# Kernel tuning notes

Measured on AMD Instinct MI355X. Metric: run time of the kernel, lower is better.

## Reference

```python
import jax, jax.numpy as jnp
import numpy as np

D_MODEL = 512
NUM_HEADS = 8
D_K = D_MODEL // NUM_HEADS


def setup_inputs() -> dict:
    key = jax.random.key(0)
    ks = jax.random.split(key, 12)
    B, Sq, Sk = 4, 2048, 2048
    scale = 1.0 / np.sqrt(D_MODEL)
    inp = {
        'query': jax.random.normal(ks[0], (B, Sq, D_MODEL), jnp.float32),
        'key':   jax.random.normal(ks[1], (B, Sk, D_MODEL), jnp.float32),
        'value': jax.random.normal(ks[2], (B, Sk, D_MODEL), jnp.float32),
        'wq': jax.random.normal(ks[3], (D_MODEL, D_MODEL), jnp.float32) * scale,
        'bq': jnp.zeros((D_MODEL,), jnp.float32),
        'wk': jax.random.normal(ks[4], (D_MODEL, D_MODEL), jnp.float32) * scale,
        'bk': jnp.zeros((D_MODEL,), jnp.float32),
        'wv': jax.random.normal(ks[5], (D_MODEL, D_MODEL), jnp.float32) * scale,
        'bv': jnp.zeros((D_MODEL,), jnp.float32),
        'wo': jax.random.normal(ks[6], (D_MODEL, D_MODEL), jnp.float32) * scale,
        'bo': jnp.zeros((D_MODEL,), jnp.float32),
        'ln_g': jnp.ones((D_MODEL,), jnp.float32),
        'ln_b': jnp.zeros((D_MODEL,), jnp.float32),
    }
    return inp


def _layer_norm(x, g, b, eps=1e-5):
    mu = jnp.mean(x, axis=-1, keepdims=True)
    var = jnp.mean(jnp.square(x - mu), axis=-1, keepdims=True)
    return (x - mu) * jax.lax.rsqrt(var + eps) * g + b


def reference(query, key, value, wq, bq, wk, bk, wv, bv, wo, bo, ln_g, ln_b):
    B, Sq, _ = query.shape
    Sk = key.shape[1]
    residual = query
    # projections: torch Linear computes x @ W^T + b; here wq is (out,in)-free:
    # we store weights as (d_model, d_model) and use x @ W + b (equivalent param space)
    Q = (query @ wq + bq).reshape(B, Sq, NUM_HEADS, D_K).transpose(0, 2, 1, 3)
    K = (key   @ wk + bk).reshape(B, Sk, NUM_HEADS, D_K).transpose(0, 2, 1, 3)
    V = (value @ wv + bv).reshape(B, Sk, NUM_HEADS, D_K).transpose(0, 2, 1, 3)
    scores = jnp.einsum('bhqd,bhkd->bhqk', Q, K) / jnp.sqrt(jnp.float32(D_K))
    attn = jax.nn.softmax(scores, axis=-1)  # dropout is identity in eval
    context = jnp.einsum('bhqk,bhkd->bhqd', attn, V)
    context = context.transpose(0, 2, 1, 3).reshape(B, Sq, D_MODEL)
    out = context @ wo + bo
    return _layer_norm(out + residual, ln_g, ln_b)
```

## Files before the change

kernel.cpp:

```cpp
#include <hip/hip_runtime.h>
#include <cstdint>
#include <cstddef>

typedef unsigned short u16;
typedef __bf16 bf16x8 __attribute__((ext_vector_type(8)));
typedef __bf16 bf16x4 __attribute__((ext_vector_type(4)));
typedef float f32x4 __attribute__((ext_vector_type(4)));

#define DEVI __device__ __forceinline__

DEVI u16 f2bf(float f){
  union { float f; unsigned u; } v; v.f = f;
  unsigned r = v.u + 0x7fffu + ((v.u >> 16) & 1u);
  return (u16)(r >> 16);
}

#if defined(__has_builtin)
#if __has_builtin(__builtin_amdgcn_exp2f)
#define EXP2F(x) __builtin_amdgcn_exp2f(x)
#else
#define EXP2F(x) exp2f(x)
#endif
#else
#define EXP2F(x) exp2f(x)
#endif

#define MFMA16(a,b,c) __builtin_amdgcn_mfma_f32_16x16x32_bf16((a),(b),(c),0,0,0)

DEVI void gload_lds16(const void* g, void* l){
  __builtin_amdgcn_global_load_lds(
      (const __attribute__((address_space(1))) void*)g,
      (__attribute__((address_space(3))) void*)l, 16, 0, 0);
}

#define BARRIER do{ __builtin_amdgcn_s_barrier(); \
    __builtin_amdgcn_sched_barrier(0); }while(0)


__global__ void k_prep_w(const float* __restrict__ w0, const float* __restrict__ w1,
                         const float* __restrict__ w2, const float* __restrict__ w3,
                         u16* __restrict__ wt){
  __shared__ u16 tile[64][72];
  int p = blockIdx.z;
  const float* W = (p==0)?w0:((p==1)?w1:((p==2)?w2:w3));
  int k0 = blockIdx.x*64, n0 = blockIdx.y*64;
  int t = threadIdx.x;
  int tr = t >> 4, tc = t & 15;
  #pragma unroll
  for (int pass=0; pass<4; pass++){
    int row = pass*16 + tr;
    float4 a = *(const float4*)(W + (size_t)(k0+row)*512 + n0 + tc*4);
    tile[row][tc*4+0] = f2bf(a.x);
    tile[row][tc*4+1] = f2bf(a.y);
    tile[row][tc*4+2] = f2bf(a.z);
    tile[row][tc*4+3] = f2bf(a.w);
  }
  __syncthreads();
  #pragma unroll
  for (int pass=0; pass<4; pass++){
    int n = pass*16 + tr;
    ushort4 o;
    o.x = tile[tc*4+0][n];
    o.y = tile[tc*4+1][n];
    o.z = tile[tc*4+2][n];
    o.w = tile[tc*4+3][n];
    *(ushort4*)(wt + (size_t)p*262144 + (size_t)(n0+n)*512 + k0 + tc*4) = o;
  }
}

__global__ __launch_bounds__(256)
void k_gemm_qkv(const float* __restrict__ xq, const float* __restrict__ xk,
                const float* __restrict__ xv, const u16* __restrict__ wt,
                const float* __restrict__ bq, const float* __restrict__ bk,
                const float* __restrict__ bv,
                u16* __restrict__ qb, u16* __restrict__ kb, u16* __restrict__ vt){
  int l = threadIdx.x & 63, w = threadIdx.x >> 6;
  int lr = l & 15, lg = l >> 4;
  int f = blockIdx.x;
  int xcd = f & 7, j0 = f >> 3;
  int pm   = xcd*24 + (j0 >> 2);
  int nblk = j0 & 3;
  int p    = pm >> 6, mblk = pm & 63;
  int wr = w >> 1, wc = w & 1;

  const float* bias = (p==0)?bq:((p==1)?bk:bv);
  float osc = (p==0)? (0.125f*1.44269504088896340736f) : 1.0f;

  const float* Ag32 = ((p==0)?xq:((p==1)?xk:xv)) + (size_t)mblk*128*512;
  const char*  Bg   = (const char*)(wt + (size_t)p*262144 + (size_t)nblk*128*512);

  __shared__ __align__(16) u16 Albuf[2][8192];
  __shared__ __align__(16) u16 Blbuf[2][8192];

  int r8 = l >> 3, sl = l & 7;
  int ar = w*8 + r8;
  int as = sl;

  float4 av[8];
  #define A_ISSUE(tt) do{ \
    _Pragma("unroll") \
    for (int p4=0; p4<4; ++p4){ \
      int r = ar + p4*32; \
      const float* src = Ag32 + (size_t)r*512 + (tt)*64 + as*8; \
      av[p4*2]   = *(const float4*)src; \
      av[p4*2+1] = *(const float4*)(src+4); \
    } }while(0)

  #define A_WRITE(buf) do{ \
    _Pragma("unroll") \
    for (int p4=0; p4<4; ++p4){ \
      int r = ar + p4*32; \
      bf16x8 o; \
      o[0]=(__bf16)av[p4*2].x;   o[1]=(__bf16)av[p4*2].y; \
      o[2]=(__bf16)av[p4*2].z;   o[3]=(__bf16)av[p4*2].w; \
      o[4]=(__bf16)av[p4*2+1].x; o[5]=(__bf16)av[p4*2+1].y; \
      o[6]=(__bf16)av[p4*2+1].z; o[7]=(__bf16)av[p4*2+1].w; \
      *(bf16x8*)((char*)Albuf[buf] + r*128 + ((as ^ (r & 7)) << 4)) = o; \
    } }while(0)

  #define B_STAGE(tt, buf) do{ \
    _Pragma("unroll") \
    for (int cc=0; cc<4; ++cc){ \
      int c = w*4 + cc; int row = c*8 + r8; \
      int sw = (sl ^ (row & 7)) << 4; \
      gload_lds16(Bg + (size_t)row*1024 + (size_t)(tt)*128 + sw, (char*)Blbuf[buf] + c*1024); \
    } }while(0)

  A_ISSUE(0);
  B_STAGE(0, 0);
  asm volatile("s_waitcnt vmcnt(4)" ::: "memory");
  A_WRITE(0);
  asm volatile("s_waitcnt lgkmcnt(0)" ::: "memory");

  f32x4 acc[4][4] = {};
  for (int t = 0; t < 8; ++t){
    int cur = t & 1;
    if (t < 7){
      A_ISSUE(t+1);
      B_STAGE(t+1, cur^1);
      asm volatile("s_waitcnt vmcnt(12)" ::: "memory");
    } else {
      asm volatile("s_waitcnt vmcnt(0)" ::: "memory");
    }
    BARRIER;
    const char* Ac = (const char*)Albuf[cur];
    const char* Bc = (const char*)Blbuf[cur];
    #pragma unroll
    for (int kk=0;kk<2;kk++){
      int ks = ((kk*4 + lg) ^ (lr & 7)) << 4;
      bf16x8 af[4], bfr[4];
      #pragma unroll
      for (int i=0;i<4;i++)
        af[i]  = *(const bf16x8*)(Ac + (wr*64 + i*16 + lr)*128 + ks);
      #pragma unroll
      for (int j=0;j<4;j++)
        bfr[j] = *(const bf16x8*)(Bc + (wc*64 + j*16 + lr)*128 + ks);
      #pragma unroll
      for (int i=0;i<4;i++)
        #pragma unroll
        for (int j=0;j<4;j++)
          acc[i][j] = MFMA16(af[i], bfr[j], acc[i][j]);
    }
    if (t < 7){
      asm volatile("s_waitcnt vmcnt(4)" ::: "memory");
      A_WRITE(cur^1);
      asm volatile("s_waitcnt lgkmcnt(0)" ::: "memory");
      BARRIER;
    }
  }
  #undef A_ISSUE
  #undef A_WRITE
  #undef B_STAGE

  int m0 = mblk*128 + wr*64;
  int n0 = nblk*128 + wc*64;
  if (p < 2){
    u16* outp = (p==0)?qb:kb;
    #pragma unroll
    for (int i=0;i<4;i++){
      #pragma unroll
      for (int j=0;j<4;j++){
        int n = n0 + j*16 + lr;
        int h = n >> 6, d = n & 63;
        float bb = bias[n];
        #pragma unroll
        for (int rg=0;rg<4;rg++){
          int m = m0 + i*16 + 4*lg + rg;
          int b = m >> 11, s = m & 2047;
          float val = (acc[i][j][rg] + bb)*osc;
          __bf16 hb = (__bf16)val;
          outp[(((size_t)b*8 + h)*2048 + s)*64 + d] = *(u16*)&hb;
        }
      }
    }
  } else {
    #pragma unroll
    for (int i=0;i<4;i++){
      #pragma unroll
      for (int j=0;j<4;j++){
        int n = n0 + j*16 + lr;
        int h = n >> 6, d = n & 63;
        float bb = bias[n];
        int m = m0 + i*16 + 4*lg;
        int b = m >> 11, s = m & 2047;
        ushort4 o;
        #pragma unroll
        for (int rg=0;rg<4;rg++){
          __bf16 hb = (__bf16)(acc[i][j][rg] + bb);
          ((u16*)&o)[rg] = *(u16*)&hb;
        }
        *(ushort4*)(vt + (((size_t)(b*8+h)*64 + d)*2048 + s)) = o;
      }
    }
  }
}

__global__ __launch_bounds__(512, 4)
void k_attn(const u16* __restrict__ qbuf, const u16* __restrict__ kbuf,
            const u16* __restrict__ vtb, u16* __restrict__ opart,
            float* __restrict__ lpart){
  int l = threadIdx.x & 63, w = threadIdx.x >> 6;
  int lr = l & 15, lg = l >> 4;
  int f = blockIdx.x;
  int bh    = (f & 7)*4 + ((f >> 3) & 3);
  int rest  = f >> 5;
  int split = rest & 1;
  int q0    = (rest >> 1)*256 + w*32;
  int b = bh >> 3, h = bh & 7;
  int kvbase = split*1024;

  const u16* Qp = qbuf + ((size_t)bh*2048 + q0)*64;
  const char* Kg = (const char*)(kbuf + (size_t)bh*2048*64) + (size_t)kvbase*128;
  const char* Vg = (const char*)(vtb  + (size_t)bh*64*2048) + (size_t)kvbase*2;

  __shared__ __align__(16) u16 Klds[3][4096];
  __shared__ __align__(16) u16 Vlds[3][4096];
  __shared__ __align__(16) u16 Plds[8][2048];
  u16* Pw = Plds[w];

  int r8 = l >> 3, sl = l & 7;

  bf16x8 qf[2][2];
  #pragma unroll
  for (int j=0;j<2;j++)
    #pragma unroll
    for (int kk=0;kk<2;kk++)
      qf[j][kk] = *(const bf16x8*)(Qp + (size_t)(j*16+lr)*64 + kk*32 + lg*8);

  bf16x8 onesf;
  #pragma unroll
  for (int e=0;e<8;e++) onesf[e] = (__bf16)1.0f;

  {
    int row = w*8 + r8;
    int sw = (sl ^ (row & 7)) << 4;
    gload_lds16(Kg + (size_t)row*128 + sw,  (char*)Klds[0] + w*1024);
    gload_lds16(Vg + (size_t)row*4096 + sw, (char*)Vlds[0] + w*1024);
  }

  f32x4 oacc[2][4] = {};
  f32x4 lacc[2] = {};

  int cur = 0;
  for (int t = 0; t < 16; ++t){
    if (t < 15){
      int nxt = (cur == 2) ? 0 : cur + 1;
      int row = w*8 + r8;
      int sw = (sl ^ (row & 7)) << 4;
      gload_lds16(Kg + (size_t)(t+1)*8192 + (size_t)row*128 + sw,
                  (char*)Klds[nxt] + w*1024);
      gload_lds16(Vg + (size_t)(t+1)*128 + (size_t)row*4096 + sw,
                  (char*)Vlds[nxt] + w*1024);
      asm volatile("s_waitcnt vmcnt(2)" ::: "memory");
    } else {
      asm volatile("s_waitcnt vmcnt(0)" ::: "memory");
    }
    BARRIER;
    const char* Kc = (const char*)Klds[cur];
    const char* Vc = (const char*)Vlds[cur];
    f32x4 sacc[4][2] = {};
    #pragma unroll
    for (int kk=0;kk<2;kk++){
      bf16x8 kf[4];
      #pragma unroll
      for (int i=0;i<4;i++)
        kf[i] = *(const bf16x8*)(Kc + (i*16+lr)*128 + (((4*kk+lg)^(lr&7))<<4));
      #pragma unroll
      for (int i=0;i<4;i++)
        #pragma unroll
        for (int j=0;j<2;j++)
          sacc[i][j] = MFMA16(kf[i], qf[j][kk], sacc[i][j]);
    }
    #pragma unroll
    for (int j=0;j<2;j++){
      int qrow = lr + 16*j;
      #pragma unroll
      for (int i=0;i<4;i++){
        bf16x4 pk;
        #pragma unroll
        for (int rg=0;rg<4;rg++)
          pk[rg] = (__bf16)EXP2F(sacc[i][j][rg]);
        int o    = 8*lg + 32*i;
        int slot = (o >> 4) ^ (qrow & 7);
        *(bf16x4*)((char*)Pw + qrow*128 + (slot<<4) + (o & 15)) = pk;
      }
    }
    #pragma unroll
    for (int kk=0;kk<2;kk++){
      bf16x8 pf[2];
      #pragma unroll
      for (int fi=0;fi<2;fi++){
        int qrow = fi*16 + lr;
        int slot = (4*kk + lg) ^ (qrow & 7);
        pf[fi] = *(const bf16x8*)((char*)Pw + qrow*128 + (slot<<4));
      }
      bf16x8 vf[4];
      #pragma unroll
      for (int fj=0;fj<4;fj++)
        vf[fj] = *(const bf16x8*)(Vc + (fj*16+lr)*128 + (((4*kk+lg)^(lr&7))<<4));
      #pragma unroll
      for (int fi=0;fi<2;fi++){
        #pragma unroll
        for (int fj=0;fj<4;fj++)
          oacc[fi][fj] = MFMA16(pf[fi], vf[fj], oacc[fi][fj]);
        lacc[fi] = MFMA16(pf[fi], onesf, lacc[fi]);
      }
    }
    cur = (cur == 2) ? 0 : cur + 1;
  }

  if (lr == 0){
    #pragma unroll
    for (int fi=0;fi<2;fi++)
      #pragma unroll
      for (int rg=0;rg<4;rg++)
        lpart[((size_t)split*32 + bh)*2048 + q0 + fi*16 + 4*lg + rg] = lacc[fi][rg];
  }
  u16* op = opart + (size_t)split*8192*512;
  #pragma unroll
  for (int fi=0;fi<2;fi++){
    #pragma unroll
    for (int fj=0;fj<4;fj++){
      int col = h*64 + fj*16 + lr;
      #pragma unroll
      for (int rg=0;rg<4;rg++){
        int qg = q0 + fi*16 + 4*lg + rg;
        __bf16 hb = (__bf16)oacc[fi][fj][rg];
        op[((size_t)(b*2048 + qg))*512 + col] = *(u16*)&hb;
      }
    }
  }
}

__global__ __launch_bounds__(256)
void k_gemm_o(const u16* __restrict__ op0, const u16* __restrict__ op1,
              const float* __restrict__ lpart, const u16* __restrict__ wto,
              u16* __restrict__ gout){
  int l = threadIdx.x & 63, w = threadIdx.x >> 6;
  int lr = l & 15, lg = l >> 4;
  int f = blockIdx.x;
  int xcd = f & 7, j0 = f >> 3;
  int mblk = xcd*16 + (j0 >> 2);
  int nblk = j0 & 3;
  int wr = w & 1, wc = w >> 1;

  int bb8 = (mblk >> 5) * 8;
  int qbase = (mblk & 31) * 64;

  const u16* Ag0 = op0 + (size_t)mblk*64*512;
  const u16* Ag1 = op1 + (size_t)mblk*64*512;
  const char* Bg = (const char*)(wto + (size_t)nblk*128*512);

  __shared__ __align__(16) u16 Albuf[2][4096];
  __shared__ __align__(16) u16 Blbuf[2][8192];

  int r8 = l >> 3, sl = l & 7;

  bf16x8 a0v[2], a1v[2]; float l0v[2], l1v[2];
  #define A_ISSUE(tt) do{ \
    _Pragma("unroll") \
    for (int cc=0; cc<2; ++cc){ \
      int c = w*2 + cc; int row = c*8 + r8; \
      int ssrc = sl ^ (row & 7); \
      a0v[cc] = *(const bf16x8*)(Ag0 + (size_t)row*512 + (tt)*64 + ssrc*8); \
      a1v[cc] = *(const bf16x8*)(Ag1 + (size_t)row*512 + (tt)*64 + ssrc*8); \
      int q = qbase + row; \
      l0v[cc] = lpart[(size_t)(bb8 + (tt))*2048 + q]; \
      l1v[cc] = lpart[(size_t)(32 + bb8 + (tt))*2048 + q]; \
    } }while(0)

  #define A_WRITE(buf) do{ \
    _Pragma("unroll") \
    for (int cc=0; cc<2; ++cc){ \
      int c = w*2 + cc; \
      float inv = 1.f / (l0v[cc] + l1v[cc]); \
      bf16x8 r; \
      _Pragma("unroll") \
      for (int e=0;e<8;e++) \
        r[e] = (__bf16)(((float)a0v[cc][e] + (float)a1v[cc][e]) * inv); \
      *(bf16x8*)((char*)Albuf[buf] + c*1024 + r8*128 + sl*16) = r; \
    } }while(0)

  #define B_STAGE(tt, buf) do{ \
    _Pragma("unroll") \
    for (int cc=0; cc<4; ++cc){ \
      int c = w*4 + cc; int row = c*8 + r8; \
      int sw = (sl ^ (row & 7)) << 4; \
      gload_lds16(Bg + (size_t)row*1024 + (size_t)(tt)*128 + sw, (char*)Blbuf[buf] + c*1024); \
    } }while(0)

  A_ISSUE(0);
  B_STAGE(0, 0);
  asm volatile("s_waitcnt vmcnt(4)" ::: "memory");
  A_WRITE(0);
  asm volatile("s_waitcnt lgkmcnt(0)" ::: "memory");

  f32x4 acc[2][4] = {};
  for (int t = 0; t < 8; ++t){
    int cur = t & 1;
    if (t < 7){
      A_ISSUE(t+1);
      B_STAGE(t+1, cur^1);
      asm volatile("s_waitcnt vmcnt(12)" ::: "memory");
    } else {
      asm volatile("s_waitcnt vmcnt(0)" ::: "memory");
    }
    BARRIER;
    const char* Ac = (const char*)Albuf[cur];
    const char* Bc = (const char*)Blbuf[cur];
    #pragma unroll
    for (int kk=0;kk<2;kk++){
      int ks = ((kk*4 + lg) ^ (lr & 7)) << 4;
      bf16x8 af[2], bfr[4];
      #pragma unroll
      for (int i=0;i<2;i++)
        af[i]  = *(const bf16x8*)(Ac + (wr*32 + i*16 + lr)*128 + ks);
      #pragma unroll
      for (int j=0;j<4;j++)
        bfr[j] = *(const bf16x8*)(Bc + (wc*64 + j*16 + lr)*128 + ks);
      #pragma unroll
      for (int i=0;i<2;i++)
        #pragma unroll
        for (int j=0;j<4;j++)
          acc[i][j] = MFMA16(af[i], bfr[j], acc[i][j]);
    }
    if (t < 7){
      asm volatile("s_waitcnt vmcnt(4)" ::: "memory");
      A_WRITE(cur^1);
      asm volatile("s_waitcnt lgkmcnt(0)" ::: "memory");
      BARRIER;
    }
  }
  #undef A_ISSUE
  #undef A_WRITE
  #undef B_STAGE

  int m0 = mblk*64 + wr*32;
  int n0 = nblk*128 + wc*64;
  #pragma unroll
  for (int i=0;i<2;i++){
    #pragma unroll
    for (int j=0;j<4;j++){
      int n = n0 + j*16 + lr;
      #pragma unroll
      for (int rg=0;rg<4;rg++){
        int m = m0 + i*16 + 4*lg + rg;
        __bf16 hb = (__bf16)acc[i][j][rg];
        gout[(size_t)m*512 + n] = *(u16*)&hb;
      }
    }
  }
}

__global__ __launch_bounds__(256)
void k_ln(const u16* __restrict__ gout, const float* __restrict__ bo,
          const float* __restrict__ resid, const float* __restrict__ g,
          const float* __restrict__ beta, float* __restrict__ out){
  int gid  = blockIdx.x*256 + threadIdx.x;
  int row  = gid >> 6;
  int lane = gid & 63;
  int c0 = lane*8;
  bf16x8 a = *(const bf16x8*)(gout + (size_t)row*512 + c0);
  float4 r0 = *(const float4*)(resid + (size_t)row*512 + c0);
  float4 r1 = *(const float4*)(resid + (size_t)row*512 + c0 + 4);
  float4 b0 = *(const float4*)(bo + c0);
  float4 b1 = *(const float4*)(bo + c0 + 4);
  float v[8];
  v[0]=(float)a[0]+b0.x+r0.x; v[1]=(float)a[1]+b0.y+r0.y;
  v[2]=(float)a[2]+b0.z+r0.z; v[3]=(float)a[3]+b0.w+r0.w;
  v[4]=(float)a[4]+b1.x+r1.x; v[5]=(float)a[5]+b1.y+r1.y;
  v[6]=(float)a[6]+b1.z+r1.z; v[7]=(float)a[7]+b1.w+r1.w;
  float s1 = 0.f, s2 = 0.f;
  #pragma unroll
  for (int e=0;e<8;e++){ s1 += v[e]; s2 += v[e]*v[e]; }
  #pragma unroll
  for (int mk=1; mk<64; mk<<=1){
    s1 += __shfl_xor(s1, mk);
    s2 += __shfl_xor(s2, mk);
  }
  float mu   = s1 * (1.f/512.f);
  float var  = s2 * (1.f/512.f) - mu*mu;
  float rstd = rsqrtf(var + 1e-5f);
  float4 g0 = *(const float4*)(g + c0);
  float4 g1 = *(const float4*)(g + c0 + 4);
  float4 e0 = *(const float4*)(beta + c0);
  float4 e1 = *(const float4*)(beta + c0 + 4);
  float4 o0, o1;
  o0.x=(v[0]-mu)*rstd*g0.x+e0.x; o0.y=(v[1]-mu)*rstd*g0.y+e0.y;
  o0.z=(v[2]-mu)*rstd*g0.z+e0.z; o0.w=(v[3]-mu)*rstd*g0.w+e0.w;
  o1.x=(v[4]-mu)*rstd*g1.x+e1.x; o1.y=(v[5]-mu)*rstd*g1.y+e1.y;
  o1.z=(v[6]-mu)*rstd*g1.z+e1.z; o1.w=(v[7]-mu)*rstd*g1.w+e1.w;
  *(float4*)(out + (size_t)row*512 + c0)     = o0;
  *(float4*)(out + (size_t)row*512 + c0 + 4) = o1;
}

extern "C" void kernel_launch(void* const* d_in, const int* in_sizes, int n_in,
                              void* d_out, int out_size, void* d_ws, size_t ws_size,
                              hipStream_t stream){
  const float* q   = (const float*)d_in[0];
  const float* k   = (const float*)d_in[1];
  const float* v   = (const float*)d_in[2];
  const float* wq  = (const float*)d_in[3];
  const float* bq  = (const float*)d_in[4];
  const float* wk  = (const float*)d_in[5];
  const float* bk  = (const float*)d_in[6];
  const float* wv  = (const float*)d_in[7];
  const float* bv  = (const float*)d_in[8];
  const float* wo  = (const float*)d_in[9];
  const float* bo  = (const float*)d_in[10];
  const float* lng = (const float*)d_in[11];
  const float* lnb = (const float*)d_in[12];
  float* out = (float*)d_out;
  char* ws = (char*)d_ws;
  u16*   wt    = (u16*)(ws + 0);
  u16*   qb    = (u16*)(ws + 2097152);
  u16*   kb    = (u16*)(ws + 10485760);
  u16*   vt    = (u16*)(ws + 18874368);
  u16*   gout  = (u16*)(ws + 27262976);
  u16*   opart = (u16*)(ws + 35651584);
  float* lpart = (float*)(ws + 52428800);

  k_prep_w<<<dim3(8,8,4), 256, 0, stream>>>(wq, wk, wv, wo, wt);
  k_gemm_qkv<<<768, 256, 0, stream>>>(q, k, v, wt, bq, bk, bv, qb, kb, vt);
  k_attn<<<512, 512, 0, stream>>>(qb, kb, vt, opart, lpart);
  k_gemm_o<<<512, 256, 0, stream>>>(opart, opart + (size_t)8192*512, lpart,
                                    wt + 3*262144, gout);
  k_ln<<<2048, 256, 0, stream>>>(gout, bo, q, lng, lnb, out);
}
```

Baseline: 99.33 us.

## Restructure QKV projection GEMM into triple-buffered 32-wide K pipeline

The QKV projection GEMM now steps over K in 32-element tiles (16 iterations) instead of 64-element tiles (8), with LDS triple-buffered and two register sets for the fp32 A prefetch, so loads run two stages ahead of compute. The LDS swizzle changes to match the 64-byte rows. The aim is to hide global load latency and cut LDS per block with one barrier per step instead of two. In exchange there are twice as many barriers and waits overall, less MFMA work between synchronisations, and more code from the fully unrolled iterations.

```diff
diff --git a/kernel.cpp b/kernel.cpp
--- a/kernel.cpp
+++ b/kernel.cpp
@@ -89,85 +89,105 @@
   const float* Ag32 = ((p==0)?xq:((p==1)?xk:xv)) + (size_t)mblk*128*512;
   const char*  Bg   = (const char*)(wt + (size_t)p*262144 + (size_t)nblk*128*512);
 
-  __shared__ __align__(16) u16 Albuf[2][8192];
-  __shared__ __align__(16) u16 Blbuf[2][8192];
-
-  int r8 = l >> 3, sl = l & 7;
-  int ar = w*8 + r8;
-  int as = sl;
-
-  float4 av[8];
-  #define A_ISSUE(tt) do{ \
-    _Pragma("unroll") \
-    for (int p4=0; p4<4; ++p4){ \
-      int r = ar + p4*32; \
-      const float* src = Ag32 + (size_t)r*512 + (tt)*64 + as*8; \
-      av[p4*2]   = *(const float4*)src; \
-      av[p4*2+1] = *(const float4*)(src+4); \
+  __shared__ __align__(16) u16 Albuf[3][4096];
+  __shared__ __align__(16) u16 Blbuf[3][4096];
+
+  int arow0 = w*32 + (l >> 2);
+  int aslot = l & 3;
+
+  #define A_ISSUE(tt, av) do{ \
+    _Pragma("unroll") \
+    for (int q=0; q<2; ++q){ \
+      int r = arow0 + q*16; \
+      const float* src = Ag32 + (size_t)r*512 + (tt)*32 + aslot*8; \
+      av[q*2]   = *(const float4*)src; \
+      av[q*2+1] = *(const float4*)(src+4); \
     } }while(0)
 
-  #define A_WRITE(buf) do{ \
-    _Pragma("unroll") \
-    for (int p4=0; p4<4; ++p4){ \
-      int r = ar + p4*32; \
+  #define A_WRITE(av, buf) do{ \
+    _Pragma("unroll") \
+    for (int q=0; q<2; ++q){ \
+      int r = arow0 + q*16; \
       bf16x8 o; \
-      o[0]=(__bf16)av[p4*2].x;   o[1]=(__bf16)av[p4*2].y; \
-      o[2]=(__bf16)av[p4*2].z;   o[3]=(__bf16)av[p4*2].w; \
-      o[4]=(__bf16)av[p4*2+1].x; o[5]=(__bf16)av[p4*2+1].y; \
-      o[6]=(__bf16)av[p4*2+1].z; o[7]=(__bf16)av[p4*2+1].w; \
-      *(bf16x8*)((char*)Albuf[buf] + r*128 + ((as ^ (r & 7)) << 4)) = o; \
+      o[0]=(__bf16)av[q*2].x;   o[1]=(__bf16)av[q*2].y; \
+      o[2]=(__bf16)av[q*2].z;   o[3]=(__bf16)av[q*2].w; \
+      o[4]=(__bf16)av[q*2+1].x; o[5]=(__bf16)av[q*2+1].y; \
+      o[6]=(__bf16)av[q*2+1].z; o[7]=(__bf16)av[q*2+1].w; \
+      *(bf16x8*)((char*)Albuf[buf] + r*64 + ((aslot ^ ((r>>1)&3))<<4)) = o; \
     } }while(0)
 
   #define B_STAGE(tt, buf) do{ \
     _Pragma("unroll") \
-    for (int cc=0; cc<4; ++cc){ \
-      int c = w*4 + cc; int row = c*8 + r8; \
-      int sw = (sl ^ (row & 7)) << 4; \
-      gload_lds16(Bg + (size_t)row*1024 + (size_t)(tt)*128 + sw, (char*)Blbuf[buf] + c*1024); \
+    for (int cc=0; cc<2; ++cc){ \
+      int c = w*2 + cc; int row = c*16 + (l>>2); \
+      int kg = (l&3) ^ ((row>>1)&3); \
+      gload_lds16(Bg + (size_t)row*1024 + (size_t)(tt)*64 + kg*16, \
+                  (char*)Blbuf[buf] + c*1024); \
     } }while(0)
 
-  A_ISSUE(0);
+  f32x4 acc[4][4] = {};
+  float4 avA[4], avB[4];
+
+  A_ISSUE(0, avA);
   B_STAGE(0, 0);
+  A_ISSUE(1, avB);
   asm volatile("s_waitcnt vmcnt(4)" ::: "memory");
-  A_WRITE(0);
+  A_WRITE(avA, 0);
   asm volatile("s_waitcnt lgkmcnt(0)" ::: "memory");
-
-  f32x4 acc[4][4] = {};
-  for (int t = 0; t < 8; ++t){
-    int cur = t & 1;
-    if (t < 7){
-      A_ISSUE(t+1);
-      B_STAGE(t+1, cur^1);
-      asm volatile("s_waitcnt vmcnt(12)" ::: "memory");
-    } else {
-      asm volatile("s_waitcnt vmcnt(0)" ::: "memory");
-    }
-    BARRIER;
-    const char* Ac = (const char*)Albuf[cur];
-    const char* Bc = (const char*)Blbuf[cur];
-    #pragma unroll
-    for (int kk=0;kk<2;kk++){
-      int ks = ((kk*4 + lg) ^ (lr & 7)) << 4;
-      bf16x8 af[4], bfr[4];
-      #pragma unroll
-      for (int i=0;i<4;i++)
-        af[i]  = *(const bf16x8*)(Ac + (wr*64 + i*16 + lr)*128 + ks);
-      #pragma unroll
-      for (int j=0;j<4;j++)
-        bfr[j] = *(const bf16x8*)(Bc + (wc*64 + j*16 + lr)*128 + ks);
-      #pragma unroll
-      for (int i=0;i<4;i++)
-        #pragma unroll
-        for (int j=0;j<4;j++)
-          acc[i][j] = MFMA16(af[i], bfr[j], acc[i][j]);
-    }
-    if (t < 7){
-      asm volatile("s_waitcnt vmcnt(4)" ::: "memory");
-      A_WRITE(cur^1);
-      asm volatile("s_waitcnt lgkmcnt(0)" ::: "memory");
-      BARRIER;
-    }
-  }
+  BARRIER;
+
+  #define QKV_COMPUTE(buf) do{ \
+    const char* Ac = (const char*)Albuf[buf]; \
+    const char* Bc = (const char*)Blbuf[buf]; \
+    bf16x8 af[4], bfr[4]; \
+    _Pragma("unroll") \
+    for (int i=0;i<4;i++){ \
+      int row = wr*64 + i*16 + lr; \
+      af[i] = *(const bf16x8*)(Ac + row*64 + ((lg ^ ((row>>1)&3))<<4)); \
+    } \
+    _Pragma("unroll") \
+    for (int j=0;j<4;j++){ \
+      int row = wc*64 + j*16 + lr; \
+      bfr[j] = *(const bf16x8*)(Bc + row*64 + ((lg ^ ((row>>1)&3))<<4)); \
+    } \
+    _Pragma("unroll") \
+    for (int i=0;i<4;i++) \
+      _Pragma("unroll") \
+      for (int j=0;j<4;j++) \
+        acc[i][j] = MFMA16(af[i], bfr[j], acc[i][j]); \
+  }while(0)
+
+  #define QKV_ITER(t, AVI, AVW) do{ \
+    if ((t) < 14) A_ISSUE((t)+2, AVI); \
+    if ((t) < 15) B_STAGE((t)+1, ((t)+1)%3); \
+    if ((t) < 14)      asm volatile("s_waitcnt vmcnt(6)" ::: "memory"); \
+    else if ((t) < 15) asm volatile("s_waitcnt vmcnt(2)" ::: "memory"); \
+    else               asm volatile("s_waitcnt vmcnt(0)" ::: "memory"); \
+    if ((t) < 15) A_WRITE(AVW, ((t)+1)%3); \
+    asm volatile("s_waitcnt lgkmcnt(0)" ::: "memory"); \
+    BARRIER; \
+    QKV_COMPUTE((t)%3); \
+  }while(0)
+
+  QKV_ITER(0,  avA, avB);
+  QKV_ITER(1,  avB, avA);
+  QKV_ITER(2,  avA, avB);
+  QKV_ITER(3,  avB, avA);
+  QKV_ITER(4,  avA, avB);
+  QKV_ITER(5,  avB, avA);
+  QKV_ITER(6,  avA, avB);
+  QKV_ITER(7,  avB, avA);
+  QKV_ITER(8,  avA, avB);
+  QKV_ITER(9,  avB, avA);
+  QKV_ITER(10, avA, avB);
+  QKV_ITER(11, avB, avA);
+  QKV_ITER(12, avA, avB);
+  QKV_ITER(13, avB, avA);
+  QKV_ITER(14, avA, avB);
+  QKV_ITER(15, avA, avA);
+
+  #undef QKV_ITER
+  #undef QKV_COMPUTE
   #undef A_ISSUE
   #undef A_WRITE
   #undef B_STAGE
```

Measured after the change: 99.66 us. Within noise of the previous version (+0.3%).
